# Kernel tuning notes

Hardware: AMD Instinct MI355X
Metric: run time of the kernel (lower is better)

The kernel has to match this reference:

```python
import jax, jax.numpy as jnp
import numpy as np

NUM_GRAPHS = 256  # B: number of graphs in the ragged batch
EMBED = 256       # input_dim / MHA embed_dim
N_NODES = 200000


def setup_inputs() -> dict:
    key = jax.random.key(0)
    k1, k2, k3, k4, k5, k6 = jax.random.split(key, 6)
    x = jax.random.normal(k1, (N_NODES, EMBED), dtype=jnp.float32)
    in_proj_w = jax.random.normal(k2, (3 * EMBED, EMBED), dtype=jnp.float32) * 0.02
    in_proj_b = jax.random.normal(k3, (3 * EMBED,), dtype=jnp.float32) * 0.02
    out_proj_w = jax.random.normal(k4, (EMBED, EMBED), dtype=jnp.float32) * 0.02
    out_proj_b = jax.random.normal(k5, (EMBED,), dtype=jnp.float32) * 0.02
    batch = jnp.sort(jax.random.randint(k6, (N_NODES,), 0, NUM_GRAPHS)).astype(jnp.int64)
    return {"x": x, "in_proj_w": in_proj_w, "in_proj_b": in_proj_b,
            "out_proj_w": out_proj_w, "out_proj_b": out_proj_b, "batch": batch}


def reference(x, in_proj_w, in_proj_b, out_proj_w, out_proj_b, batch):
    E = x.shape[1]
    # global_mean_pool: per-graph mean of node features -> [B, E]
    sums = jax.ops.segment_sum(x, batch, num_segments=NUM_GRAPHS)
    counts = jax.ops.segment_sum(jnp.ones((x.shape[0],), x.dtype), batch,
                                 num_segments=NUM_GRAPHS)
    g = sums / jnp.maximum(counts, 1.0)[:, None]  # [B, E]
    # MultiheadAttention with a single K/V vector per graph: softmax over S=1
    # is identically 1, so attention output = out_proj(V_proj(g)) for every
    # query node of that graph (Q path contributes nothing).
    Wv = in_proj_w[2 * E:3 * E]
    bv = in_proj_b[2 * E:3 * E]
    v = g @ Wv.T + bv                       # [B, E] value projection
    out_graph = v @ out_proj_w.T + out_proj_b  # [B, E] output projection
    # broadcast back to nodes (torch.cat over per-graph slices)
    return out_graph[batch]                 # [N, E]
```

## Files before the change

### kernel.cpp

```cpp
#include <hip/hip_runtime.h>

#define EMBED   256
#define NGRAPH  256
#define K1_CHUNK 512

__global__ __launch_bounds__(256) void seg_sum_kernel(
    const float* __restrict__ x, const int* __restrict__ batch,
    float* __restrict__ sums, int nNodes) {
  __shared__ int sb[K1_CHUNK];
  const int start = blockIdx.x * K1_CHUNK;
  const int cnt = min(K1_CHUNK, nNodes - start);
  for (int i = threadIdx.x; i < cnt; i += 256) sb[i] = batch[start + i];
  __syncthreads();

  const int q = threadIdx.x >> 6;
  const int c = (threadIdx.x & 63) << 2;
  float4 acc = make_float4(0.f, 0.f, 0.f, 0.f);
  int cur = -1;
  for (int i = q; i < cnt; i += 4) {
    const int g = sb[i];
    const float4 v = *(const float4*)(x + (size_t)(start + i) * EMBED + c);
    if (g != cur) {
      if (cur >= 0) {
        float* p = sums + (size_t)cur * EMBED + c;
        atomicAdd(p + 0, acc.x); atomicAdd(p + 1, acc.y);
        atomicAdd(p + 2, acc.z); atomicAdd(p + 3, acc.w);
      }
      acc = make_float4(0.f, 0.f, 0.f, 0.f);
      cur = g;
    }
    acc.x += v.x; acc.y += v.y; acc.z += v.z; acc.w += v.w;
  }
  if (cur >= 0) {
    float* p = sums + (size_t)cur * EMBED + c;
    atomicAdd(p + 0, acc.x); atomicAdd(p + 1, acc.y);
    atomicAdd(p + 2, acc.z); atomicAdd(p + 3, acc.w);
  }
}

__global__ __launch_bounds__(256) void mlp_kernel(
    const float* __restrict__ sums, const int* __restrict__ batch,
    const float* __restrict__ in_w, const float* __restrict__ in_b,
    const float* __restrict__ out_w, const float* __restrict__ out_b,
    float* __restrict__ out_graph, int nNodes) {
  const int g = blockIdx.x;
  const int t = threadIdx.x;

  int lo = 0, hi = nNodes;
  while (lo < hi) { int m = (lo + hi) >> 1; (batch[m] <  g) ? (lo = m + 1) : (hi = m); }
  int lo2 = lo, hi2 = nNodes;
  while (lo2 < hi2) { int m = (lo2 + hi2) >> 1; (batch[m] <= g) ? (lo2 = m + 1) : (hi2 = m); }
  const float inv = 1.0f / fmaxf((float)(lo2 - lo), 1.0f);

  __shared__ float sg[EMBED];
  __shared__ float sv[EMBED];
  sg[t] = sums[(size_t)g * EMBED + t] * inv;
  __syncthreads();

  const float* Wv = in_w + 2 * EMBED * EMBED;
  float acc = in_b[2 * EMBED + t];
  const float4* wrow = (const float4*)(Wv + (size_t)t * EMBED);
#pragma unroll 8
  for (int k4 = 0; k4 < EMBED / 4; ++k4) {
    const float4 w = wrow[k4];
    const int k = k4 * 4;
    acc += sg[k] * w.x + sg[k + 1] * w.y + sg[k + 2] * w.z + sg[k + 3] * w.w;
  }
  sv[t] = acc;
  __syncthreads();

  float acc2 = out_b[t];
  const float4* w2row = (const float4*)(out_w + (size_t)t * EMBED);
#pragma unroll 8
  for (int k4 = 0; k4 < EMBED / 4; ++k4) {
    const float4 w = w2row[k4];
    const int k = k4 * 4;
    acc2 += sv[k] * w.x + sv[k + 1] * w.y + sv[k + 2] * w.z + sv[k + 3] * w.w;
  }
  out_graph[(size_t)g * EMBED + t] = acc2;
}

__global__ __launch_bounds__(256) void gather_kernel(
    const float* __restrict__ out_graph, const int* __restrict__ batch,
    float4* __restrict__ out, int nNodes) {
  const int i = blockIdx.x * 256 + threadIdx.x;
  const int total = nNodes * (EMBED / 4);
  if (i >= total) return;
  const int n = i >> 6;
  const int c = i & 63;
  const int g = batch[n];
  out[i] = ((const float4*)out_graph)[g * (EMBED / 4) + c];
}

extern "C" void kernel_launch(void* const* d_in, const int* in_sizes, int n_in,
                              void* d_out, int out_size, void* d_ws, size_t ws_size,
                              hipStream_t stream) {
  const float* x     = (const float*)d_in[0];
  const float* in_w  = (const float*)d_in[1];
  const float* in_b  = (const float*)d_in[2];
  const float* out_w = (const float*)d_in[3];
  const float* out_b = (const float*)d_in[4];
  const int*   batch = (const int*)d_in[5];
  const int nNodes = in_sizes[5];

  float* sums      = (float*)d_ws;
  float* out_graph = sums + (size_t)NGRAPH * EMBED;

  hipMemsetAsync(sums, 0, (size_t)NGRAPH * EMBED * sizeof(float), stream);

  const int nb1 = (nNodes + K1_CHUNK - 1) / K1_CHUNK;
  seg_sum_kernel<<<nb1, 256, 0, stream>>>(x, batch, sums, nNodes);

  mlp_kernel<<<NGRAPH, 256, 0, stream>>>(sums, batch, in_w, in_b, out_w, out_b,
                                         out_graph, nNodes);

  const int nb3 = (nNodes * (EMBED / 4) + 255) / 256;
  gather_kernel<<<nb3, 256, 0, stream>>>(out_graph, batch, (float4*)d_out, nNodes);
}
```

Before: 418.8 us.

## Fuse segment sum, MLP and broadcast into one per-graph kernel

Replaces the memset, atomic segment-sum, MLP and gather kernels with one kernel that runs one 512-thread block per graph. Each block binary-searches its node range, reduces x rows directly without atomics, applies both projections in shared memory, and writes the result to its node range without reading batch again. This removes three launches, the atomics and the per-node batch lookup. The cost is that only 256 blocks must stream the whole input and output, which may limit memory parallelism on a 256-CU part.

```diff
diff --git a/kernel.cpp b/kernel.cpp
--- a/kernel.cpp
+++ b/kernel.cpp
@@ -2,94 +2,107 @@
 
 #define EMBED   256
 #define NGRAPH  256
-#define K1_CHUNK 512
+#define NW      8
+#define BLOCK   (NW * 64)
 
-__global__ __launch_bounds__(256) void seg_sum_kernel(
+__global__ __launch_bounds__(BLOCK, 1) void fused_kernel(
     const float* __restrict__ x, const int* __restrict__ batch,
-    float* __restrict__ sums, int nNodes) {
-  __shared__ int sb[K1_CHUNK];
-  const int start = blockIdx.x * K1_CHUNK;
-  const int cnt = min(K1_CHUNK, nNodes - start);
-  for (int i = threadIdx.x; i < cnt; i += 256) sb[i] = batch[start + i];
+    const float* __restrict__ in_w, const float* __restrict__ in_b,
+    const float* __restrict__ out_w, const float* __restrict__ out_b,
+    float* __restrict__ out, int nNodes) {
+  const int g = blockIdx.x;
+  const int t = threadIdx.x;
+  const int q  = t >> 6;
+  const int c4 = t & 63;
+
+  int n0, n1;
+  { int a = 0, b = nNodes;
+    while (a < b) { int m = (a + b) >> 1; (batch[m] < g) ? (a = m + 1) : (b = m); }
+    n0 = a; }
+  { int a = n0, b = nNodes;
+    while (a < b) { int m = (a + b) >> 1; (batch[m] <= g) ? (a = m + 1) : (b = m); }
+    n1 = a; }
+  const int cnt = n1 - n0;
+
+  const float4* xp = (const float4*)x + (size_t)n0 * (EMBED / 4) + c4;
+  float4 a0 = make_float4(0.f, 0.f, 0.f, 0.f);
+  float4 a1 = make_float4(0.f, 0.f, 0.f, 0.f);
+  int i = q;
+  for (; i + 7 * NW < cnt; i += 8 * NW) {
+    float4 v0 = xp[(size_t)(i         ) * (EMBED / 4)];
+    float4 v1 = xp[(size_t)(i + 1 * NW) * (EMBED / 4)];
+    float4 v2 = xp[(size_t)(i + 2 * NW) * (EMBED / 4)];
+    float4 v3 = xp[(size_t)(i + 3 * NW) * (EMBED / 4)];
+    float4 v4 = xp[(size_t)(i + 4 * NW) * (EMBED / 4)];
+    float4 v5 = xp[(size_t)(i + 5 * NW) * (EMBED / 4)];
+    float4 v6 = xp[(size_t)(i + 6 * NW) * (EMBED / 4)];
+    float4 v7 = xp[(size_t)(i + 7 * NW) * (EMBED / 4)];
+    a0.x += v0.x + v1.x; a0.y += v0.y + v1.y; a0.z += v0.z + v1.z; a0.w += v0.w + v1.w;
+    a1.x += v2.x + v3.x; a1.y += v2.y + v3.y; a1.z += v2.z + v3.z; a1.w += v2.w + v3.w;
+    a0.x += v4.x + v5.x; a0.y += v4.y + v5.y; a0.z += v4.z + v5.z; a0.w += v4.w + v5.w;
+    a1.x += v6.x + v7.x; a1.y += v6.y + v7.y; a1.z += v6.z + v7.z; a1.w += v6.w + v7.w;
+  }
+  for (; i < cnt; i += NW) {
+    float4 v = xp[(size_t)i * (EMBED / 4)];
+    a0.x += v.x; a0.y += v.y; a0.z += v.z; a0.w += v.w;
+  }
+  a0.x += a1.x; a0.y += a1.y; a0.z += a1.z; a0.w += a1.w;
+
+  __shared__ float4 red4[NW][EMBED / 4];
+  __shared__ float sg[EMBED];
+  __shared__ float sv[EMBED];
+  __shared__ float so[EMBED];
+  red4[q][c4] = a0;
   __syncthreads();
 
-  const int q = threadIdx.x >> 6;
-  const int c = (threadIdx.x & 63) << 2;
-  float4 acc = make_float4(0.f, 0.f, 0.f, 0.f);
-  int cur = -1;
-  for (int i = q; i < cnt; i += 4) {
-    const int g = sb[i];
-    const float4 v = *(const float4*)(x + (size_t)(start + i) * EMBED + c);
-    if (g != cur) {
-      if (cur >= 0) {
-        float* p = sums + (size_t)cur * EMBED + c;
-        atomicAdd(p + 0, acc.x); atomicAdd(p + 1, acc.y);
-        atomicAdd(p + 2, acc.z); atomicAdd(p + 3, acc.w);
-      }
-      acc = make_float4(0.f, 0.f, 0.f, 0.f);
-      cur = g;
-    }
-    acc.x += v.x; acc.y += v.y; acc.z += v.z; acc.w += v.w;
+  const float inv = 1.0f / fmaxf((float)cnt, 1.0f);
+  if (t < EMBED) {
+    const float* rf = (const float*)red4;
+    float s = 0.f;
+#pragma unroll
+    for (int k = 0; k < NW; ++k) s += rf[k * EMBED + t];
+    sg[t] = s * inv;
   }
-  if (cur >= 0) {
-    float* p = sums + (size_t)cur * EMBED + c;
-    atomicAdd(p + 0, acc.x); atomicAdd(p + 1, acc.y);
-    atomicAdd(p + 2, acc.z); atomicAdd(p + 3, acc.w);
-  }
-}
-
-__global__ __launch_bounds__(256) void mlp_kernel(
-    const float* __restrict__ sums, const int* __restrict__ batch,
-    const float* __restrict__ in_w, const float* __restrict__ in_b,
-    const float* __restrict__ out_w, const float* __restrict__ out_b,
-    float* __restrict__ out_graph, int nNodes) {
-  const int g = blockIdx.x;
-  const int t = threadIdx.x;
-
-  int lo = 0, hi = nNodes;
-  while (lo < hi) { int m = (lo + hi) >> 1; (batch[m] <  g) ? (lo = m + 1) : (hi = m); }
-  int lo2 = lo, hi2 = nNodes;
-  while (lo2 < hi2) { int m = (lo2 + hi2) >> 1; (batch[m] <= g) ? (lo2 = m + 1) : (hi2 = m); }
-  const float inv = 1.0f / fmaxf((float)(lo2 - lo), 1.0f);
-
-  __shared__ float sg[EMBED];
-  __shared__ float sv[EMBED];
-  sg[t] = sums[(size_t)g * EMBED + t] * inv;
   __syncthreads();
 
-  const float* Wv = in_w + 2 * EMBED * EMBED;
-  float acc = in_b[2 * EMBED + t];
-  const float4* wrow = (const float4*)(Wv + (size_t)t * EMBED);
+  if (t < EMBED) {
+    float acc = in_b[2 * EMBED + t];
+    const float4* wrow = (const float4*)(in_w + (size_t)(2 * EMBED + t) * EMBED);
 #pragma unroll 8
-  for (int k4 = 0; k4 < EMBED / 4; ++k4) {
-    const float4 w = wrow[k4];
-    const int k = k4 * 4;
-    acc += sg[k] * w.x + sg[k + 1] * w.y + sg[k + 2] * w.z + sg[k + 3] * w.w;
+    for (int k4 = 0; k4 < EMBED / 4; ++k4) {
+      const float4 w = wrow[k4];
+      const int k = k4 * 4;
+      acc += sg[k] * w.x + sg[k + 1] * w.y + sg[k + 2] * w.z + sg[k + 3] * w.w;
+    }
+    sv[t] = acc;
   }
-  sv[t] = acc;
   __syncthreads();
 
-  float acc2 = out_b[t];
-  const float4* w2row = (const float4*)(out_w + (size_t)t * EMBED);
+  if (t < EMBED) {
+    float acc = out_b[t];
+    const float4* wrow = (const float4*)(out_w + (size_t)t * EMBED);
 #pragma unroll 8
-  for (int k4 = 0; k4 < EMBED / 4; ++k4) {
-    const float4 w = w2row[k4];
-    const int k = k4 * 4;
-    acc2 += sv[k] * w.x + sv[k + 1] * w.y + sv[k + 2] * w.z + sv[k + 3] * w.w;
+    for (int k4 = 0; k4 < EMBED / 4; ++k4) {
+      const float4 w = wrow[k4];
+      const int k = k4 * 4;
+      acc += sv[k] * w.x + sv[k + 1] * w.y + sv[k + 2] * w.z + sv[k + 3] * w.w;
+    }
+    so[t] = acc;
   }
-  out_graph[(size_t)g * EMBED + t] = acc2;
-}
+  __syncthreads();
 
-__global__ __launch_bounds__(256) void gather_kernel(
-    const float* __restrict__ out_graph, const int* __restrict__ batch,
-    float4* __restrict__ out, int nNodes) {
-  const int i = blockIdx.x * 256 + threadIdx.x;
-  const int total = nNodes * (EMBED / 4);
-  if (i >= total) return;
-  const int n = i >> 6;
-  const int c = i & 63;
-  const int g = batch[n];
-  out[i] = ((const float4*)out_graph)[g * (EMBED / 4) + c];
+  const float4 oval = ((const float4*)so)[c4];
+  float4* op = (float4*)out + c4;
+  int n = n0 + q;
+  for (; n + 3 * NW < n1; n += 4 * NW) {
+    op[(size_t)(n         ) * (EMBED / 4)] = oval;
+    op[(size_t)(n + 1 * NW) * (EMBED / 4)] = oval;
+    op[(size_t)(n + 2 * NW) * (EMBED / 4)] = oval;
+    op[(size_t)(n + 3 * NW) * (EMBED / 4)] = oval;
+  }
+  for (; n < n1; n += NW) {
+    op[(size_t)n * (EMBED / 4)] = oval;
+  }
 }
 
 extern "C" void kernel_launch(void* const* d_in, const int* in_sizes, int n_in,
@@ -103,17 +116,6 @@
   const int*   batch = (const int*)d_in[5];
   const int nNodes = in_sizes[5];
 
-  float* sums      = (float*)d_ws;
-  float* out_graph = sums + (size_t)NGRAPH * EMBED;
-
-  hipMemsetAsync(sums, 0, (size_t)NGRAPH * EMBED * sizeof(float), stream);
-
-  const int nb1 = (nNodes + K1_CHUNK - 1) / K1_CHUNK;
-  seg_sum_kernel<<<nb1, 256, 0, stream>>>(x, batch, sums, nNodes);
-
-  mlp_kernel<<<NGRAPH, 256, 0, stream>>>(sums, batch, in_w, in_b, out_w, out_b,
-                                         out_graph, nNodes);
-
-  const int nb3 = (nNodes * (EMBED / 4) + 255) / 256;
-  gather_kernel<<<nb3, 256, 0, stream>>>(out_graph, batch, (float4*)d_out, nNodes);
+  fused_kernel<<<NGRAPH, BLOCK, 0, stream>>>(x, batch, in_w, in_b, out_w, out_b,
+                                             (float*)d_out, nNodes);
 }
```

New measurement: 376.4 us. 1.11x faster.

## Replace atomic segment-sum with per-chunk partials reduced in MLP kernel

Applied to the files above, without the earlier changes.

The segment sum now writes per-wave partial sums plus graph ids into a workspace instead of issuing float atomics. Chunks are smaller, uniform chunks use an unrolled fast path, and x is read with nontemporal loads. The MLP kernel gathers the partials belonging to each graph, which also removes the memset. The gather kernel uses nontemporal stores. This adds a partials buffer and a scan over slots in the MLP kernel, and a chunk wave that meets more than MAXG graphs would drop sums, though that is unlikely with sorted batches.

```diff
diff --git a/kernel.cpp b/kernel.cpp
--- a/kernel.cpp
+++ b/kernel.cpp
@@ -1,65 +1,107 @@
 #include <hip/hip_runtime.h>
 
-#define EMBED   256
-#define NGRAPH  256
-#define K1_CHUNK 512
+#define EMBED  256
+#define NGRAPH 256
+#define CH     128
+#define MAXG   4
 
-__global__ __launch_bounds__(256) void seg_sum_kernel(
+typedef __attribute__((ext_vector_type(4))) float f4;
+
+__global__ __launch_bounds__(256, 8) void k1_partial(
     const float* __restrict__ x, const int* __restrict__ batch,
-    float* __restrict__ sums, int nNodes) {
-  __shared__ int sb[K1_CHUNK];
-  const int start = blockIdx.x * K1_CHUNK;
-  const int cnt = min(K1_CHUNK, nNodes - start);
-  for (int i = threadIdx.x; i < cnt; i += 256) sb[i] = batch[start + i];
+    f4* __restrict__ part, int* __restrict__ pgid, int nNodes) {
+  __shared__ int sb[CH];
+  const int blk   = blockIdx.x;
+  const int start = blk * CH;
+  const int cnt   = min(CH, nNodes - start);
+  const int t     = threadIdx.x;
+  if (t < cnt) sb[t] = batch[start + t];
   __syncthreads();
 
-  const int q = threadIdx.x >> 6;
-  const int c = (threadIdx.x & 63) << 2;
-  float4 acc = make_float4(0.f, 0.f, 0.f, 0.f);
-  int cur = -1;
-  for (int i = q; i < cnt; i += 4) {
-    const int g = sb[i];
-    const float4 v = *(const float4*)(x + (size_t)(start + i) * EMBED + c);
-    if (g != cur) {
-      if (cur >= 0) {
-        float* p = sums + (size_t)cur * EMBED + c;
-        atomicAdd(p + 0, acc.x); atomicAdd(p + 1, acc.y);
-        atomicAdd(p + 2, acc.z); atomicAdd(p + 3, acc.w);
+  const int q    = t >> 6;
+  const int lane = t & 63;
+  const f4* xp   = (const f4*)x + (size_t)start * 64 + lane;
+  const int slot0 = (blk * 4 + q) * MAXG;
+
+  f4 acc = (f4){0.f, 0.f, 0.f, 0.f};
+
+  if (cnt == CH && sb[0] == sb[CH - 1]) {
+#pragma unroll
+    for (int k = 0; k < 32; k += 8) {
+      f4 v0 = __builtin_nontemporal_load(xp + (size_t)((k + 0) * 4 + q) * 64);
+      f4 v1 = __builtin_nontemporal_load(xp + (size_t)((k + 1) * 4 + q) * 64);
+      f4 v2 = __builtin_nontemporal_load(xp + (size_t)((k + 2) * 4 + q) * 64);
+      f4 v3 = __builtin_nontemporal_load(xp + (size_t)((k + 3) * 4 + q) * 64);
+      f4 v4 = __builtin_nontemporal_load(xp + (size_t)((k + 4) * 4 + q) * 64);
+      f4 v5 = __builtin_nontemporal_load(xp + (size_t)((k + 5) * 4 + q) * 64);
+      f4 v6 = __builtin_nontemporal_load(xp + (size_t)((k + 6) * 4 + q) * 64);
+      f4 v7 = __builtin_nontemporal_load(xp + (size_t)((k + 7) * 4 + q) * 64);
+      acc += (v0 + v1) + (v2 + v3) + ((v4 + v5) + (v6 + v7));
+    }
+    part[(size_t)slot0 * 64 + lane] = acc;
+    if (lane == 0) {
+      pgid[slot0 + 0] = sb[0];
+      pgid[slot0 + 1] = -1; pgid[slot0 + 2] = -1; pgid[slot0 + 3] = -1;
+    }
+  } else {
+    int m = 0, cur = -1;
+    for (int i = q; i < cnt; i += 4) {
+      const int g = sb[i];
+      if (g != cur) {
+        if (cur >= 0 && m < MAXG) {
+          part[(size_t)(slot0 + m) * 64 + lane] = acc;
+          if (lane == 0) pgid[slot0 + m] = cur;
+          m++;
+        }
+        acc = (f4){0.f, 0.f, 0.f, 0.f};
+        cur = g;
       }
-      acc = make_float4(0.f, 0.f, 0.f, 0.f);
-      cur = g;
+      acc += __builtin_nontemporal_load(xp + (size_t)i * 64);
     }
-    acc.x += v.x; acc.y += v.y; acc.z += v.z; acc.w += v.w;
-  }
-  if (cur >= 0) {
-    float* p = sums + (size_t)cur * EMBED + c;
-    atomicAdd(p + 0, acc.x); atomicAdd(p + 1, acc.y);
-    atomicAdd(p + 2, acc.z); atomicAdd(p + 3, acc.w);
+    if (cur >= 0 && m < MAXG) {
+      part[(size_t)(slot0 + m) * 64 + lane] = acc;
+      if (lane == 0) pgid[slot0 + m] = cur;
+      m++;
+    }
+    if (lane == 0)
+      for (int s = m; s < MAXG; ++s) pgid[slot0 + s] = -1;
   }
 }
 
-__global__ __launch_bounds__(256) void mlp_kernel(
-    const float* __restrict__ sums, const int* __restrict__ batch,
+__global__ __launch_bounds__(256) void k2_mlp(
+    const int* __restrict__ batch,
+    const f4* __restrict__ part, const int* __restrict__ pgid,
     const float* __restrict__ in_w, const float* __restrict__ in_b,
     const float* __restrict__ out_w, const float* __restrict__ out_b,
-    float* __restrict__ out_graph, int nNodes) {
+    float* __restrict__ rows, int nNodes) {
   const int g = blockIdx.x;
   const int t = threadIdx.x;
 
-  int lo = 0, hi = nNodes;
-  while (lo < hi) { int m = (lo + hi) >> 1; (batch[m] <  g) ? (lo = m + 1) : (hi = m); }
-  int lo2 = lo, hi2 = nNodes;
-  while (lo2 < hi2) { int m = (lo2 + hi2) >> 1; (batch[m] <= g) ? (lo2 = m + 1) : (hi2 = m); }
-  const float inv = 1.0f / fmaxf((float)(lo2 - lo), 1.0f);
+  int n0, n1;
+  { int a = 0, b = nNodes;
+    while (a < b) { int m = (a + b) >> 1; (batch[m] <  g) ? (a = m + 1) : (b = m); }
+    n0 = a; }
+  { int a = n0, b = nNodes;
+    while (a < b) { int m = (a + b) >> 1; (batch[m] <= g) ? (a = m + 1) : (b = m); }
+    n1 = a; }
+  const int cnt = n1 - n0;
+
+  float s = 0.f;
+  if (cnt > 0) {
+    const int b0 = n0 / CH, b1 = (n1 - 1) / CH;
+    const float* pf = (const float*)part;
+    for (int r = b0 * 4 * MAXG; r < (b1 + 1) * 4 * MAXG; ++r) {
+      if (pgid[r] == g) s += pf[(size_t)r * EMBED + t];
+    }
+  }
 
   __shared__ float sg[EMBED];
   __shared__ float sv[EMBED];
-  sg[t] = sums[(size_t)g * EMBED + t] * inv;
+  sg[t] = s / fmaxf((float)cnt, 1.0f);
   __syncthreads();
 
-  const float* Wv = in_w + 2 * EMBED * EMBED;
   float acc = in_b[2 * EMBED + t];
-  const float4* wrow = (const float4*)(Wv + (size_t)t * EMBED);
+  const float4* wrow = (const float4*)(in_w + (size_t)(2 * EMBED + t) * EMBED);
 #pragma unroll 8
   for (int k4 = 0; k4 < EMBED / 4; ++k4) {
     const float4 w = wrow[k4];
@@ -77,19 +119,19 @@
     const int k = k4 * 4;
     acc2 += sv[k] * w.x + sv[k + 1] * w.y + sv[k + 2] * w.z + sv[k + 3] * w.w;
   }
-  out_graph[(size_t)g * EMBED + t] = acc2;
+  rows[(size_t)g * EMBED + t] = acc2;
 }
 
-__global__ __launch_bounds__(256) void gather_kernel(
-    const float* __restrict__ out_graph, const int* __restrict__ batch,
-    float4* __restrict__ out, int nNodes) {
+__global__ __launch_bounds__(256) void k3_gather(
+    const float* __restrict__ rows, const int* __restrict__ batch,
+    f4* __restrict__ out, int nNodes) {
   const int i = blockIdx.x * 256 + threadIdx.x;
-  const int total = nNodes * (EMBED / 4);
-  if (i >= total) return;
   const int n = i >> 6;
   const int c = i & 63;
+  if (n >= nNodes) return;
   const int g = batch[n];
-  out[i] = ((const float4*)out_graph)[g * (EMBED / 4) + c];
+  const f4 v = ((const f4*)rows)[g * 64 + c];
+  __builtin_nontemporal_store(v, out + i);
 }
 
 extern "C" void kernel_launch(void* const* d_in, const int* in_sizes, int n_in,
@@ -103,17 +145,18 @@
   const int*   batch = (const int*)d_in[5];
   const int nNodes = in_sizes[5];
 
-  float* sums      = (float*)d_ws;
-  float* out_graph = sums + (size_t)NGRAPH * EMBED;
+  const int nb = (nNodes + CH - 1) / CH;
+  const int nSlots = nb * 4 * MAXG;
 
-  hipMemsetAsync(sums, 0, (size_t)NGRAPH * EMBED * sizeof(float), stream);
+  f4*    part = (f4*)d_ws;
+  float* rows = (float*)(part + (size_t)nSlots * 64);
+  int*   pgid = (int*)(rows + (size_t)NGRAPH * EMBED);
 
-  const int nb1 = (nNodes + K1_CHUNK - 1) / K1_CHUNK;
-  seg_sum_kernel<<<nb1, 256, 0, stream>>>(x, batch, sums, nNodes);
+  k1_partial<<<nb, 256, 0, stream>>>(x, batch, part, pgid, nNodes);
 
-  mlp_kernel<<<NGRAPH, 256, 0, stream>>>(sums, batch, in_w, in_b, out_w, out_b,
-                                         out_graph, nNodes);
+  k2_mlp<<<NGRAPH, 256, 0, stream>>>(batch, part, pgid, in_w, in_b,
+                                     out_w, out_b, rows, nNodes);
 
-  const int nb3 = (nNodes * (EMBED / 4) + 255) / 256;
-  gather_kernel<<<nb3, 256, 0, stream>>>(out_graph, batch, (float4*)d_out, nNodes);
+  const int nb3 = (nNodes * 64 + 255) / 256;
+  k3_gather<<<nb3, 256, 0, stream>>>(rows, batch, (f4*)d_out, nNodes);
 }
```

Result: faster. 383.5 us (-8.4%).
